# Performance work log

Measured on AMD Instinct MI355X. Metric: run time of the kernel, lower is better.

The kernel has to match this reference:

```python
import jax, jax.numpy as jnp
import numpy as np

NEG = -1000000000.0

def setup_inputs() -> dict:
    key = jax.random.key(0)
    k1, k2 = jax.random.split(key)
    N, D, K = 8192, 4096, 64
    z = jax.random.normal(k1, (N, D), dtype=jnp.float32)
    W = jax.random.normal(k2, (K, D), dtype=jnp.float32) * (1.0 / np.sqrt(D))
    b = jnp.zeros((K,), dtype=jnp.float32)
    return {"z": z, "W": W, "b": b, "k": 2}

def reference(z, W, b, k):
    # logits: [N, K]
    logits = jnp.einsum('nd,kd->nk', z, W) + b
    _, topk_idx = jax.lax.top_k(logits, k)  # [N, k]
    N = logits.shape[0]
    rows = jnp.arange(N)[:, None]
    mask = jnp.zeros_like(logits).at[rows, topk_idx].set(1.0)
    sparse_logits = logits + NEG * (1.0 - mask)
    alpha = jax.nn.softmax(sparse_logits, axis=-1)
    return alpha
```

## Files before the change

kernel.cpp:

```cpp
#include <hip/hip_runtime.h>
#include <math.h>


typedef _Float16 f16x8 __attribute__((ext_vector_type(8)));
typedef _Float16 f16x4 __attribute__((ext_vector_type(4)));
typedef float    f32x4 __attribute__((ext_vector_type(4)));

constexpr int D_DIM  = 4096;
constexpr int K_DIM  = 64;
constexpr int BM     = 64;
constexpr int CH     = 128;
constexpr int KQ     = 8;
constexpr int KRANGE = D_DIM / KQ;
constexpr int NCH    = KRANGE / CH;
constexpr int BLOCK  = 512;
constexpr int LSTR   = 136;

__global__ __launch_bounds__(256) void prep_w(
    const float* __restrict__ W, _Float16* __restrict__ Wf0,
    _Float16* __restrict__ Wf1)
{
    int f = blockIdx.x * 256 + threadIdx.x;
    const float4 v = *(const float4*)(W + (long)f * 4);
    const float* p = (const float*)&v;
    f16x4 h, l;
#pragma unroll
    for (int j = 0; j < 4; ++j) {
        _Float16 hh = (_Float16)p[j];
        h[j] = hh;
        l[j] = (_Float16)((p[j] - (float)hh) * 2048.0f);
    }
    *(f16x4*)(Wf0 + (long)f * 4) = h;
    *(f16x4*)(Wf1 + (long)f * 4) = l;
}

__global__ __launch_bounds__(BLOCK, 6) void gemm_f16limb(
    const float* __restrict__ z, const _Float16* __restrict__ Wf0,
    const _Float16* __restrict__ Wf1, float* __restrict__ part, int N)
{
    __shared__ __align__(16) _Float16 Az[2][BM][LSTR];

    const int tid  = threadIdx.x;
    const int lane = tid & 63;
    const int wv   = tid >> 6;
    const int mt   = wv >> 1;
    const int nh   = wv & 1;
    const int m16  = lane & 15;
    const int quad = lane >> 4;

    const int rgrp  = blockIdx.x >> 3;
    const int kq    = blockIdx.x & 7;
    const long m0   = (long)rgrp * BM;
    const int kbase = kq * KRANGE;

    float4 zb[4];
#pragma unroll
    for (int i = 0; i < 4; ++i) {
        int f = tid + i * BLOCK, r = f >> 5, c4 = (f & 31) * 4;
        zb[i] = *(const float4*)(z + (m0 + r) * (long)D_DIM + kbase + c4);
    }

    f32x4 acch[2], accl[2];
#pragma unroll
    for (int t = 0; t < 2; ++t) {
        acch[t] = (f32x4){0.f, 0.f, 0.f, 0.f};
        accl[t] = (f32x4){0.f, 0.f, 0.f, 0.f};
    }

    for (int ch = 0; ch < NCH; ++ch) {
#pragma unroll
        for (int i = 0; i < 4; ++i) {
            int f = tid + i * BLOCK, r = f >> 5, c4 = (f & 31) * 4;
            const float* p = (const float*)&zb[i];
            f16x4 h, l;
#pragma unroll
            for (int j = 0; j < 4; ++j) {
                _Float16 hh = (_Float16)p[j];
                h[j] = hh;
                l[j] = (_Float16)((p[j] - (float)hh) * 2048.0f);
            }
            *(f16x4*)&Az[0][r][c4] = h;
            *(f16x4*)&Az[1][r][c4] = l;
        }
        if (ch + 1 < NCH) {
            const int k0 = kbase + (ch + 1) * CH;
#pragma unroll
            for (int i = 0; i < 4; ++i) {
                int f = tid + i * BLOCK, r = f >> 5, c4 = (f & 31) * 4;
                zb[i] = *(const float4*)(z + (m0 + r) * (long)D_DIM + k0 + c4);
            }
        }
        __syncthreads();

        const int mrow = mt * 16 + m16;
#pragma unroll
        for (int ks2 = 0; ks2 < 4; ++ks2) {
            const int klocal = ks2 * 32 + quad * 8;
            const long kglob = kbase + ch * CH + klocal;
            const f16x8 ah = *(const f16x8*)&Az[0][mrow][klocal];
            const f16x8 al = *(const f16x8*)&Az[1][mrow][klocal];
#pragma unroll
            for (int t = 0; t < 2; ++t) {
                const int n = (nh * 2 + t) * 16 + m16;
                const f16x8 bh = *(const f16x8*)(Wf0 + (long)n * D_DIM + kglob);
                const f16x8 bl = *(const f16x8*)(Wf1 + (long)n * D_DIM + kglob);
                accl[t] = __builtin_amdgcn_mfma_f32_16x16x32_f16(al, bh, accl[t], 0, 0, 0);
                accl[t] = __builtin_amdgcn_mfma_f32_16x16x32_f16(ah, bl, accl[t], 0, 0, 0);
                acch[t] = __builtin_amdgcn_mfma_f32_16x16x32_f16(ah, bh, acch[t], 0, 0, 0);
            }
        }
        __syncthreads();
    }

#pragma unroll
    for (int t = 0; t < 2; ++t) {
#pragma unroll
        for (int r = 0; r < 4; ++r) {
            long row = m0 + mt * 16 + quad * 4 + r;
            int  col = (nh * 2 + t) * 16 + m16;
            part[((long)kq * N + row) * K_DIM + col] =
                acch[t][r] + accl[t][r] * 4.8828125e-4f;
        }
    }
}

constexpr int RG2  = 32;
constexpr int BLK2 = 256;

__global__ __launch_bounds__(BLK2) void reduce_topk(
    const float* __restrict__ part, const float* __restrict__ bias,
    float* __restrict__ out, int N)
{
    __shared__ float lg[RG2][K_DIM + 1];
    __shared__ float sa1[RG2], sa2[RG2];
    __shared__ int   si1[RG2], si2[RG2];

    const int tid = threadIdx.x;
    const long r0 = (long)blockIdx.x * RG2;

#pragma unroll
    for (int i = 0; i < (RG2 * K_DIM) / (BLK2 * 4); ++i) {
        int f = tid + i * BLK2, r = f >> 4, c4 = (f & 15) * 4;
        float4 s = *(const float4*)(part + (r0 + r) * K_DIM + c4);
#pragma unroll
        for (int q = 1; q < KQ; ++q) {
            const float4 v = *(const float4*)(part + ((long)q * N + r0 + r) * K_DIM + c4);
            s.x += v.x; s.y += v.y; s.z += v.z; s.w += v.w;
        }
        const float4 bv = *(const float4*)(bias + c4);
        lg[r][c4 + 0] = s.x + bv.x;
        lg[r][c4 + 1] = s.y + bv.y;
        lg[r][c4 + 2] = s.z + bv.z;
        lg[r][c4 + 3] = s.w + bv.w;
    }
    __syncthreads();

    if (tid < RG2) {
        float m1 = -INFINITY, m2 = -INFINITY;
        int i1 = 0, i2 = 0;
        for (int j = 0; j < K_DIM; ++j) {
            float v = lg[tid][j];
            if (v > m1)      { m2 = m1; i2 = i1; m1 = v; i1 = j; }
            else if (v > m2) { m2 = v; i2 = j; }
        }
        float e2  = expf(m2 - m1);
        float inv = 1.f / (1.f + e2);
        sa1[tid] = inv; sa2[tid] = e2 * inv;
        si1[tid] = i1;  si2[tid] = i2;
    }
    __syncthreads();

    float* obase = out + r0 * K_DIM;
#pragma unroll
    for (int i = 0; i < (RG2 * K_DIM) / (BLK2 * 4); ++i) {
        int f = tid + i * BLK2, r = f >> 4, j = (f & 15) * 4;
        int i1 = si1[r], i2 = si2[r];
        float a1 = sa1[r], a2 = sa2[r];
        float4 v;
        v.x = (j + 0 == i1) ? a1 : ((j + 0 == i2) ? a2 : 0.f);
        v.y = (j + 1 == i1) ? a1 : ((j + 1 == i2) ? a2 : 0.f);
        v.z = (j + 2 == i1) ? a1 : ((j + 2 == i2) ? a2 : 0.f);
        v.w = (j + 3 == i1) ? a1 : ((j + 3 == i2) ? a2 : 0.f);
        *(float4*)(obase + (long)r * K_DIM + j) = v;
    }
}

extern "C" void kernel_launch(void* const* d_in, const int* in_sizes, int n_in,
                              void* d_out, int out_size, void* d_ws, size_t ws_size,
                              hipStream_t stream) {
    const float* z = (const float*)d_in[0];
    const float* W = (const float*)d_in[1];
    const float* b = (const float*)d_in[2];
    float* out  = (float*)d_out;
    const int N = in_sizes[0] / D_DIM;

    float*    part = (float*)d_ws;
    _Float16* Wf0  = (_Float16*)((char*)d_ws + ((size_t)24 << 20));
    _Float16* Wf1  = Wf0 + (size_t)K_DIM * D_DIM;

    prep_w      <<<dim3((K_DIM * D_DIM / 4) / 256), dim3(256), 0, stream>>>(W, Wf0, Wf1);
    gemm_f16limb<<<dim3((N / BM) * KQ), dim3(BLOCK), 0, stream>>>(z, Wf0, Wf1, part, N);
    reduce_topk <<<dim3(N / RG2),       dim3(BLK2), 0, stream>>>(part, b, out, N);
}
```

Measured before the change: 256.2 us.

## Stage W limbs in LDS and stream z directly to registers without barriers

The GEMM now loads the block's W high/low fp16 limbs into shared memory once. Each wave then streams its own 16 rows of z straight from global memory into registers, with one-step double buffering and on-the-fly fp16 limb splitting, so the main loop has no __syncthreads. The row tile grows to 128 and the K split to 16, which doubles the partial-sum buffer that reduce_topk must write and read back. The workspace offset for the W limbs is moved to make room for the larger buffer. Per-lane z loads are narrower, so global-load latency is less hidden than with the earlier cooperative LDS staging.

```diff
diff --git a/kernel.cpp b/kernel.cpp
--- a/kernel.cpp
+++ b/kernel.cpp
@@ -8,13 +8,11 @@
 
 constexpr int D_DIM  = 4096;
 constexpr int K_DIM  = 64;
-constexpr int BM     = 64;
-constexpr int CH     = 128;
-constexpr int KQ     = 8;
+constexpr int BM     = 128;
+constexpr int KQ     = 16;
 constexpr int KRANGE = D_DIM / KQ;
-constexpr int NCH    = KRANGE / CH;
 constexpr int BLOCK  = 512;
-constexpr int LSTR   = 136;
+constexpr int BSTR   = 264;
 
 __global__ __launch_bounds__(256) void prep_w(
     const float* __restrict__ W, _Float16* __restrict__ Wf0,
@@ -34,92 +32,80 @@
     *(f16x4*)(Wf1 + (long)f * 4) = l;
 }
 
-__global__ __launch_bounds__(BLOCK, 6) void gemm_f16limb(
+__global__ __launch_bounds__(BLOCK, 4) void gemm_nobar(
     const float* __restrict__ z, const _Float16* __restrict__ Wf0,
     const _Float16* __restrict__ Wf1, float* __restrict__ part, int N)
 {
-    __shared__ __align__(16) _Float16 Az[2][BM][LSTR];
+    __shared__ __align__(16) _Float16 Bs[2][K_DIM][BSTR];
 
     const int tid  = threadIdx.x;
     const int lane = tid & 63;
     const int wv   = tid >> 6;
-    const int mt   = wv >> 1;
-    const int nh   = wv & 1;
     const int m16  = lane & 15;
     const int quad = lane >> 4;
 
-    const int rgrp  = blockIdx.x >> 3;
-    const int kq    = blockIdx.x & 7;
+    const int rgrp  = blockIdx.x >> 4;
+    const int kq    = blockIdx.x & 15;
     const long m0   = (long)rgrp * BM;
     const int kbase = kq * KRANGE;
 
-    float4 zb[4];
 #pragma unroll
-    for (int i = 0; i < 4; ++i) {
-        int f = tid + i * BLOCK, r = f >> 5, c4 = (f & 31) * 4;
-        zb[i] = *(const float4*)(z + (m0 + r) * (long)D_DIM + kbase + c4);
+    for (int i = 0; i < 8; ++i) {
+        int f  = tid + i * BLOCK;
+        int p  = f >> 11;
+        int rr = (f >> 5) & 63;
+        int c  = f & 31;
+        const _Float16* src = (p ? Wf1 : Wf0) + (long)rr * D_DIM + kbase + c * 8;
+        *(f16x8*)&Bs[p][rr][c * 8] = *(const f16x8*)src;
+    }
+    __syncthreads();
+
+    const float* zp = z + (m0 + wv * 16 + m16) * (long)D_DIM + kbase;
+
+    f32x4 acch[4], accl[4];
+#pragma unroll
+    for (int nt = 0; nt < 4; ++nt) {
+        acch[nt] = (f32x4){0.f, 0.f, 0.f, 0.f};
+        accl[nt] = (f32x4){0.f, 0.f, 0.f, 0.f};
     }
 
-    f32x4 acch[2], accl[2];
+    float4 za[2][2];
+    za[0][0] = *(const float4*)(zp + quad * 8);
+    za[0][1] = *(const float4*)(zp + quad * 8 + 4);
+
 #pragma unroll
-    for (int t = 0; t < 2; ++t) {
-        acch[t] = (f32x4){0.f, 0.f, 0.f, 0.f};
-        accl[t] = (f32x4){0.f, 0.f, 0.f, 0.f};
-    }
-
-    for (int ch = 0; ch < NCH; ++ch) {
+    for (int s = 0; s < KRANGE / 32; ++s) {
+        const int cur = s & 1;
+        if (s + 1 < KRANGE / 32) {
+            za[cur ^ 1][0] = *(const float4*)(zp + (s + 1) * 32 + quad * 8);
+            za[cur ^ 1][1] = *(const float4*)(zp + (s + 1) * 32 + quad * 8 + 4);
+        }
+        f16x8 ah, al;
+        const float* pz = (const float*)&za[cur][0];
 #pragma unroll
-        for (int i = 0; i < 4; ++i) {
-            int f = tid + i * BLOCK, r = f >> 5, c4 = (f & 31) * 4;
-            const float* p = (const float*)&zb[i];
-            f16x4 h, l;
+        for (int j = 0; j < 8; ++j) {
+            _Float16 hh = (_Float16)pz[j];
+            ah[j] = hh;
+            al[j] = (_Float16)((pz[j] - (float)hh) * 2048.0f);
+        }
+        const int ko = s * 32 + quad * 8;
 #pragma unroll
-            for (int j = 0; j < 4; ++j) {
-                _Float16 hh = (_Float16)p[j];
-                h[j] = hh;
-                l[j] = (_Float16)((p[j] - (float)hh) * 2048.0f);
-            }
-            *(f16x4*)&Az[0][r][c4] = h;
-            *(f16x4*)&Az[1][r][c4] = l;
+        for (int nt = 0; nt < 4; ++nt) {
+            const f16x8 bh = *(const f16x8*)&Bs[0][nt * 16 + m16][ko];
+            const f16x8 bl = *(const f16x8*)&Bs[1][nt * 16 + m16][ko];
+            accl[nt] = __builtin_amdgcn_mfma_f32_16x16x32_f16(al, bh, accl[nt], 0, 0, 0);
+            accl[nt] = __builtin_amdgcn_mfma_f32_16x16x32_f16(ah, bl, accl[nt], 0, 0, 0);
+            acch[nt] = __builtin_amdgcn_mfma_f32_16x16x32_f16(ah, bh, acch[nt], 0, 0, 0);
         }
-        if (ch + 1 < NCH) {
-            const int k0 = kbase + (ch + 1) * CH;
-#pragma unroll
-            for (int i = 0; i < 4; ++i) {
-                int f = tid + i * BLOCK, r = f >> 5, c4 = (f & 31) * 4;
-                zb[i] = *(const float4*)(z + (m0 + r) * (long)D_DIM + k0 + c4);
-            }
-        }
-        __syncthreads();
-
-        const int mrow = mt * 16 + m16;
-#pragma unroll
-        for (int ks2 = 0; ks2 < 4; ++ks2) {
-            const int klocal = ks2 * 32 + quad * 8;
-            const long kglob = kbase + ch * CH + klocal;
-            const f16x8 ah = *(const f16x8*)&Az[0][mrow][klocal];
-            const f16x8 al = *(const f16x8*)&Az[1][mrow][klocal];
-#pragma unroll
-            for (int t = 0; t < 2; ++t) {
-                const int n = (nh * 2 + t) * 16 + m16;
-                const f16x8 bh = *(const f16x8*)(Wf0 + (long)n * D_DIM + kglob);
-                const f16x8 bl = *(const f16x8*)(Wf1 + (long)n * D_DIM + kglob);
-                accl[t] = __builtin_amdgcn_mfma_f32_16x16x32_f16(al, bh, accl[t], 0, 0, 0);
-                accl[t] = __builtin_amdgcn_mfma_f32_16x16x32_f16(ah, bl, accl[t], 0, 0, 0);
-                acch[t] = __builtin_amdgcn_mfma_f32_16x16x32_f16(ah, bh, acch[t], 0, 0, 0);
-            }
-        }
-        __syncthreads();
     }
 
 #pragma unroll
-    for (int t = 0; t < 2; ++t) {
+    for (int nt = 0; nt < 4; ++nt) {
 #pragma unroll
         for (int r = 0; r < 4; ++r) {
-            long row = m0 + mt * 16 + quad * 4 + r;
-            int  col = (nh * 2 + t) * 16 + m16;
-            part[((long)kq * N + row) * K_DIM + col] =
-                acch[t][r] + accl[t][r] * 4.8828125e-4f;
+            long row = m0 + wv * 16 + quad * 4 + r;
+            part[((long)kq * N + row) * K_DIM + nt * 16 + m16] =
+                acch[nt][r] + accl[nt][r] * 4.8828125e-4f;
         }
     }
 }
@@ -195,10 +181,10 @@
     const int N = in_sizes[0] / D_DIM;
 
     float*    part = (float*)d_ws;
-    _Float16* Wf0  = (_Float16*)((char*)d_ws + ((size_t)24 << 20));
+    _Float16* Wf0  = (_Float16*)((char*)d_ws + ((size_t)64 << 20));
     _Float16* Wf1  = Wf0 + (size_t)K_DIM * D_DIM;
 
-    prep_w      <<<dim3((K_DIM * D_DIM / 4) / 256), dim3(256), 0, stream>>>(W, Wf0, Wf1);
-    gemm_f16limb<<<dim3((N / BM) * KQ), dim3(BLOCK), 0, stream>>>(z, Wf0, Wf1, part, N);
-    reduce_topk <<<dim3(N / RG2),       dim3(BLK2), 0, stream>>>(part, b, out, N);
+    prep_w     <<<dim3((K_DIM * D_DIM / 4) / 256), dim3(256), 0, stream>>>(W, Wf0, Wf1);
+    gemm_nobar <<<dim3((N / BM) * KQ), dim3(BLOCK), 0, stream>>>(z, Wf0, Wf1, part, N);
+    reduce_topk<<<dim3(N / RG2),       dim3(BLK2), 0, stream>>>(part, b, out, N);
 }
```

Measured after the change: 215.4 us. 1.19x faster.
